# Kernel optimization log

Measured on AMD Instinct MI355X. Metric: run time of the kernel, lower is better.

## Reference

```python
import jax, jax.numpy as jnp
import numpy as np

B, T, C, H = 4, 2048, 768, 12
HD = C // H  # 64
EPS = 1e-5


def layer_norm(x, g, b):
    mu = jnp.mean(x, axis=-1, keepdims=True)
    var = jnp.var(x, axis=-1, keepdims=True)
    return (x - mu) * jax.lax.rsqrt(var + EPS) * g + b


def setup_inputs() -> dict:
    key = jax.random.key(0)
    ks = jax.random.split(key, 14)
    s_c = 1.0 / np.sqrt(C)
    s_4c = 1.0 / np.sqrt(4 * C)
    return {
        "x": jax.random.normal(ks[0], (B, T, C), jnp.float32),
        # per-head Q/K/V projections stacked over heads [H, C, HD]
        "wq": jax.random.uniform(ks[1], (H, C, HD), jnp.float32, -s_c, s_c),
        "bq": jnp.zeros((H, HD), jnp.float32),
        "wk": jax.random.uniform(ks[2], (H, C, HD), jnp.float32, -s_c, s_c),
        "bk": jnp.zeros((H, HD), jnp.float32),
        "wv": jax.random.uniform(ks[3], (H, C, HD), jnp.float32, -s_c, s_c),
        "bv": jnp.zeros((H, HD), jnp.float32),
        "w_proj": jax.random.uniform(ks[4], (C, C), jnp.float32, -s_c, s_c),
        "b_proj": jnp.zeros((C,), jnp.float32),
        "w1": jax.random.uniform(ks[5], (C, 4 * C), jnp.float32, -s_c, s_c),
        "b1": jnp.zeros((4 * C,), jnp.float32),
        "w2": jax.random.uniform(ks[6], (4 * C, C), jnp.float32, -s_4c, s_4c),
        "b2": jnp.zeros((C,), jnp.float32),
        "g1": jnp.ones((C,), jnp.float32),
        "beta1": jnp.zeros((C,), jnp.float32),
        "g2": jnp.ones((C,), jnp.float32),
        "beta2": jnp.zeros((C,), jnp.float32),
    }


def reference(x, wq, bq, wk, bk, wv, bv, w_proj, b_proj, w1, b1, w2, b2, g1, beta1, g2, beta2):
    # --- attention sublayer ---
    h = layer_norm(x, g1, beta1)
    q = jnp.einsum('btc,hcd->bhtd', h, wq) + bq[None, :, None, :]
    k = jnp.einsum('btc,hcd->bhtd', h, wk) + bk[None, :, None, :]
    v = jnp.einsum('btc,hcd->bhtd', h, wv) + bv[None, :, None, :]
    # NOTE: source applies NO 1/sqrt(head_size) scaling
    scores = jnp.einsum('bhtd,bhsd->bhts', q, k)  # [B,H,T,T]
    causal = jnp.tril(jnp.ones((T, T), bool))
    scores = jnp.where(causal, scores, -jnp.inf)
    wei = jax.nn.softmax(scores, axis=-1)
    attn = jnp.einsum('bhts,bhsd->bhtd', wei, v)  # [B,H,T,HD]
    attn = attn.transpose(0, 2, 1, 3).reshape(B, T, C)  # concat heads
    x = x + attn @ w_proj + b_proj
    # --- MLP sublayer ---
    h2 = layer_norm(x, g2, beta2)
    x = x + jax.nn.relu(h2 @ w1 + b1) @ w2 + b2
    return x
```

## Files before the change

### kernel.cpp

```cpp
#include <hip/hip_runtime.h>
#include <hip/hip_bf16.h>
#include <math.h>

#define BB 4
#define TT 2048
#define CC 768
#define HH 12
#define HDIM 64
#define C4 3072
#define MM (BB*TT)
#define EPSL 1e-5f

typedef __bf16 bf16x8 __attribute__((ext_vector_type(8)));
typedef __bf16 bf16x4 __attribute__((ext_vector_type(4)));
typedef float f32x4 __attribute__((ext_vector_type(4)));

__device__ __forceinline__ ushort f2bf(float f) {
    union { float f; unsigned u; } v; v.f = f;
    unsigned r = v.u + 0x7fffu + ((v.u >> 16) & 1u);
    return (ushort)(r >> 16);
}

__device__ __forceinline__ void glds16(const void* g, void* l) {
    __builtin_amdgcn_global_load_lds(
        (const __attribute__((address_space(1))) void*)g,
        (__attribute__((address_space(3))) void*)l, 16, 0, 0);
}

#define WVM(N) asm volatile("s_waitcnt vmcnt(" #N ")" ::: "memory")
#define WLG0   asm volatile("s_waitcnt lgkmcnt(0)" ::: "memory")

__device__ __forceinline__ void pbar() {
    __builtin_amdgcn_sched_barrier(0);
    __builtin_amdgcn_s_barrier();
    __builtin_amdgcn_sched_barrier(0);
}

__global__ __launch_bounds__(256) void ln_k(const float* __restrict__ X,
                                            const float* __restrict__ G,
                                            const float* __restrict__ Be,
                                            ushort* __restrict__ O)
{
    int row = blockIdx.x;
    const float* xr = X + (size_t)row * CC;
    int t = threadIdx.x;
    float v0 = xr[t], v1 = xr[t + 256], v2 = xr[t + 512];
    float s  = v0 + v1 + v2;
    float sq = v0*v0 + v1*v1 + v2*v2;
    #pragma unroll
    for (int off = 32; off; off >>= 1) {
        s  += __shfl_xor(s,  off);
        sq += __shfl_xor(sq, off);
    }
    __shared__ float red[8];
    int wv = t >> 6, ln = t & 63;
    if (ln == 0) { red[wv] = s; red[4 + wv] = sq; }
    __syncthreads();
    s  = red[0] + red[1] + red[2] + red[3];
    sq = red[4] + red[5] + red[6] + red[7];
    float mu  = s * (1.0f / CC);
    float var = sq * (1.0f / CC) - mu * mu;
    float rs  = rsqrtf(var + EPSL);
    ushort* orow = O + (size_t)row * CC;
    orow[t]       = f2bf((v0 - mu) * rs * G[t]       + Be[t]);
    orow[t + 256] = f2bf((v1 - mu) * rs * G[t + 256] + Be[t + 256]);
    orow[t + 512] = f2bf((v2 - mu) * rs * G[t + 512] + Be[t + 512]);
}

__global__ __launch_bounds__(256) void ln_add_k(float* __restrict__ X,
                                                const float* __restrict__ P,
                                                const float* __restrict__ G,
                                                const float* __restrict__ Be,
                                                ushort* __restrict__ O)
{
    int row = blockIdx.x;
    float* xr = X + (size_t)row * CC;
    const float* pr = P + (size_t)row * CC;
    int t = threadIdx.x;
    float v0 = xr[t]       + pr[t];
    float v1 = xr[t + 256] + pr[t + 256];
    float v2 = xr[t + 512] + pr[t + 512];
    xr[t] = v0; xr[t + 256] = v1; xr[t + 512] = v2;
    float s  = v0 + v1 + v2;
    float sq = v0*v0 + v1*v1 + v2*v2;
    #pragma unroll
    for (int off = 32; off; off >>= 1) {
        s  += __shfl_xor(s,  off);
        sq += __shfl_xor(sq, off);
    }
    __shared__ float red[8];
    int wv = t >> 6, ln = t & 63;
    if (ln == 0) { red[wv] = s; red[4 + wv] = sq; }
    __syncthreads();
    s  = red[0] + red[1] + red[2] + red[3];
    sq = red[4] + red[5] + red[6] + red[7];
    float mu  = s * (1.0f / CC);
    float var = sq * (1.0f / CC) - mu * mu;
    float rs  = rsqrtf(var + EPSL);
    ushort* orow = O + (size_t)row * CC;
    orow[t]       = f2bf((v0 - mu) * rs * G[t]       + Be[t]);
    orow[t + 256] = f2bf((v1 - mu) * rs * G[t + 256] + Be[t + 256]);
    orow[t + 512] = f2bf((v2 - mu) * rs * G[t + 512] + Be[t + 512]);
}

__global__ __launch_bounds__(256) void addto_k(float* __restrict__ o,
                                               const float* __restrict__ p,
                                               int n4)
{
    int i = blockIdx.x * 256 + threadIdx.x;
    int stride = gridDim.x * 256;
    for (; i < n4; i += stride) {
        float4 a = ((const float4*)o)[i];
        float4 b = ((const float4*)p)[i];
        a.x += b.x; a.y += b.y; a.z += b.z; a.w += b.w;
        ((float4*)o)[i] = a;
    }
}

__global__ __launch_bounds__(256) void repack_all_k(
    const float* __restrict__ wq, const float* __restrict__ wk,
    const float* __restrict__ wvw, const float* __restrict__ wp,
    const float* __restrict__ w1, const float* __restrict__ w2,
    ushort* __restrict__ WTqkv, ushort* __restrict__ WTp,
    ushort* __restrict__ WT1, ushort* __restrict__ WT2)
{
    __shared__ float tl[64][65];
    int blk = blockIdx.x;
    const float* W; ushort* WT;
    int N, outStride, nbx, local, mode;
    if (blk < 576) {
        int wsel = blk / 144; local = blk - wsel * 144; nbx = 12;
        N = 768; outStride = 768;
        mode = wsel < 3 ? 1 : 0;
        W  = wsel == 0 ? wq : (wsel == 1 ? wk : (wsel == 2 ? wvw : wp));
        WT = wsel == 3 ? WTp : WTqkv + (size_t)wsel * 768 * 768;
    } else if (blk < 1152) {
        local = blk - 576; nbx = 48; N = 3072; outStride = 768; mode = 0;
        W = w1; WT = WT1;
    } else {
        local = blk - 1152; nbx = 12; N = 768; outStride = 3072; mode = 0;
        W = w2; WT = WT2;
    }
    int n0 = (local % nbx) * 64, k0 = (local / nbx) * 64;
    int c = threadIdx.x & 63, rr = threadIdx.x >> 6;
    #pragma unroll
    for (int i = 0; i < 16; ++i) {
        int r = i * 4 + rr;
        float v;
        if (mode == 0) v = W[(size_t)(k0 + r) * N + n0 + c];
        else           v = W[((size_t)(n0 >> 6) * CC + k0 + r) * 64 + c];
        tl[r][c] = v;
    }
    __syncthreads();
    #pragma unroll
    for (int i = 0; i < 16; ++i) {
        int r = i * 4 + rr;
        WT[(size_t)(n0 + r) * outStride + k0 + c] = f2bf(tl[c][r]);
    }
}

template<int EPI>
__global__ __launch_bounds__(512, 3) void gemm3s(
    const ushort* __restrict__ A, const ushort* __restrict__ BT,
    int M, int N, int K,
    void* __restrict__ ov0, void* __restrict__ ov1, void* __restrict__ ov2,
    const float* __restrict__ bias0, const float* __restrict__ bias1,
    const float* __restrict__ bias2,
    const float* __restrict__ resid, ushort* __restrict__ obf,
    float* __restrict__ part)
{
    __shared__ ushort lds[3 * 12288];

    int nbx = gridDim.x;
    int nwg = nbx * gridDim.y * gridDim.z;
    int orig = (blockIdx.z * gridDim.y + blockIdx.y) * nbx + blockIdx.x;
    int cpx = nwg >> 3;
    int swz = (orig & 7) * cpx + (orig >> 3);
    int zi = swz / (nbx * gridDim.y);
    int rem = swz - zi * nbx * gridDim.y;
    int bn = rem % nbx, bm = rem / nbx;

    int tid = threadIdx.x;
    int lane = tid & 63;
    int w = tid >> 6;
    int wrow = (w >> 2) * 64, wcol = (w & 3) * 64;
    int fr = lane & 15, kh = lane >> 4;
    int rxor = ((fr >> 1) & 3) * 8;

    const size_t aR0 = (size_t)bm * 128;
    const size_t bR0 = (size_t)bn * 256;
    const int Ksl = K / (int)gridDim.z;
    const int koff = zi * Ksl;
    const int nt = Ksl >> 5;

    int srow = tid >> 2;
    int scol = (tid & 3) * 8;
    int sxor = scol ^ (((tid >> 3) & 3) * 8);

    f32x4 acc[4][4] = {};

    auto stage = [&](int slot, int t) {
        int kb = koff + (t << 5) + sxor;
        ushort* As = lds + slot * 12288;
        glds16(A  + (aR0 + srow) * K + kb,       As + srow * 32 + scol);
        glds16(BT + (bR0 + srow) * K + kb,       As + 4096 + srow * 32 + scol);
        glds16(BT + (bR0 + 128 + srow) * K + kb, As + 4096 + (128 + srow) * 32 + scol);
    };

    stage(0, 0);
    stage(1, 1);
    WVM(3);
    pbar();

    int slot = 0;
    for (int t = 0; t < nt; ++t) {
        const ushort* As = lds + slot * 12288;
        const ushort* Bs = As + 4096;
        bf16x8 aF[4], bF[4];
        #pragma unroll
        for (int i = 0; i < 4; ++i)
            aF[i] = *(const bf16x8*)&As[(wrow + i * 16 + fr) * 32 + ((kh * 8) ^ rxor)];
        #pragma unroll
        for (int j = 0; j < 4; ++j)
            bF[j] = *(const bf16x8*)&Bs[(wcol + j * 16 + fr) * 32 + ((kh * 8) ^ rxor)];
        if (t + 2 < nt) {
            int ns = slot + 2; if (ns >= 3) ns -= 3;
            stage(ns, t + 2);
        }
        __builtin_amdgcn_s_setprio(1);
        #pragma unroll
        for (int i = 0; i < 4; ++i)
            #pragma unroll
            for (int j = 0; j < 4; ++j)
                acc[i][j] = __builtin_amdgcn_mfma_f32_16x16x32_bf16(aF[i], bF[j], acc[i][j], 0, 0, 0);
        __builtin_amdgcn_s_setprio(0);
        if (t + 2 < nt) { WVM(3); } else { WVM(0); }
        WLG0;
        pbar();
        slot = slot + 1 == 3 ? 0 : slot + 1;
    }

    if (gridDim.z > 1 && zi > 0) {
        #pragma unroll
        for (int i = 0; i < 4; ++i) {
            int row0 = bm * 128 + wrow + i * 16 + kh * 4;
            #pragma unroll
            for (int j = 0; j < 4; ++j) {
                int col = bn * 256 + wcol + j * 16 + fr;
                #pragma unroll
                for (int r = 0; r < 4; ++r)
                    part[(size_t)(row0 + r) * N + col] = acc[i][j][r];
            }
        }
    } else if (EPI == 1) {
        int seg = bn / 3;
        ushort* op = (ushort*)(seg == 0 ? ov0 : (seg == 1 ? ov1 : ov2));
        const float* bsp = seg == 0 ? bias0 : (seg == 1 ? bias1 : bias2);
        int cb = (bn - seg * 3) * 256 + wcol;
        int h = cb >> 6;
        #pragma unroll
        for (int i = 0; i < 4; ++i) {
            int row0 = bm * 128 + wrow + i * 16 + kh * 4;
            int b = row0 >> 11;
            int t0 = row0 & (TT - 1);
            #pragma unroll
            for (int j = 0; j < 4; ++j) {
                int d = j * 16 + fr;
                float bsv = bsp[h * 64 + d];
                #pragma unroll
                for (int r = 0; r < 4; ++r)
                    op[((size_t)(b * HH + h) * TT + t0 + r) * 64 + d] =
                        f2bf(acc[i][j][r] + bsv);
            }
        }
    } else if (EPI == 2) {
        float* o0 = (float*)ov0;
        #pragma unroll
        for (int i = 0; i < 4; ++i) {
            int row0 = bm * 128 + wrow + i * 16 + kh * 4;
            #pragma unroll
            for (int j = 0; j < 4; ++j) {
                int col = bn * 256 + wcol + j * 16 + fr;
                float bsv = bias0[col];
                #pragma unroll
                for (int r = 0; r < 4; ++r) {
                    size_t idx = (size_t)(row0 + r) * N + col;
                    o0[idx] = acc[i][j][r] + bsv + resid[idx];
                }
            }
        }
    } else {
        #pragma unroll
        for (int i = 0; i < 4; ++i) {
            int row0 = bm * 128 + wrow + i * 16 + kh * 4;
            #pragma unroll
            for (int j = 0; j < 4; ++j) {
                int col = bn * 256 + wcol + j * 16 + fr;
                float bsv = bias0[col];
                #pragma unroll
                for (int r = 0; r < 4; ++r) {
                    float v = fmaxf(acc[i][j][r] + bsv, 0.f);
                    obf[(size_t)(row0 + r) * N + col] = f2bf(v);
                }
            }
        }
    }
}

__global__ __launch_bounds__(256) void vtrans_k(const ushort* __restrict__ V,
                                                ushort* __restrict__ Vt)
{
    __shared__ ushort tl[64][72];
    int blk = blockIdx.x;
    int tt = blk & 31, bh = blk >> 5;
    size_t base = (size_t)bh * TT * 64;
    int t0 = tt * 64;
    int e = threadIdx.x;
    int rr = e >> 3, cc8 = (e & 7) * 8;
    #pragma unroll
    for (int p = 0; p < 2; ++p) {
        int t = p * 32 + rr;
        *(uint4*)&tl[t][cc8] = *(const uint4*)&V[base + (size_t)(t0 + t) * 64 + cc8];
    }
    __syncthreads();
    #pragma unroll
    for (int p = 0; p < 2; ++p) {
        int d = p * 32 + rr;
        ushort tmp[8];
        #pragma unroll
        for (int i = 0; i < 8; ++i) tmp[i] = tl[cc8 + i][d];
        *(uint4*)&Vt[base + (size_t)d * TT + t0 + cc8] = *(uint4*)tmp;
    }
}

__global__ __launch_bounds__(256) void attn_k(const ushort* __restrict__ Q,
                                              const ushort* __restrict__ Kb,
                                              const ushort* __restrict__ Vt,
                                              ushort* __restrict__ Ob)
{
    __shared__ ushort Kl[2][64][64];
    __shared__ ushort Vl[2][64][64];
    __shared__ ushort Pl[4][16][68];

    int orig = blockIdx.x;
    int swz = (orig & 7) * 96 + (orig >> 3);
    int pair = swz & 15;
    int bh = swz >> 4;
    int b = bh / HH, h = bh - b * HH;
    int tid = threadIdx.x, lane = tid & 63, w = tid >> 6;
    int c = lane & 15, g = lane >> 4;
    size_t base = (size_t)bh * TT * 64;
    int srow = tid >> 3;
    int scol = (tid & 7) * 8;
    int sw0 = scol ^ ((srow & 7) * 8);
    int sw1 = scol ^ (((srow + 32) & 7) * 8);
    int rxk = (c & 7) * 8;
    const float LOG2E = 1.44269504088896340736f;

    #pragma unroll
    for (int sel = 0; sel < 2; ++sel) {
        int qt = sel ? (31 - pair) : pair;
        int q0 = qt * 64;
        int nt = qt + 1;

        bf16x8 aq[2];
        #pragma unroll
        for (int kc = 0; kc < 2; ++kc) {
            bf16x8 raw = *(const bf16x8*)&Q[base + (size_t)(q0 + w * 16 + c) * 64 + kc * 32 + g * 8];
            #pragma unroll
            for (int e = 0; e < 8; ++e)
                raw[e] = (__bf16)((float)raw[e] * LOG2E);
            aq[kc] = raw;
        }

        f32x4 oa[4] = {};
        float mrun[4] = {-INFINITY, -INFINITY, -INFINITY, -INFINITY};
        float lrun[4] = {0.f, 0.f, 0.f, 0.f};

        {
            uint4 a0 = *(const uint4*)&Kb[base + (size_t)srow * 64 + scol];
            uint4 a1 = *(const uint4*)&Kb[base + (size_t)(32 + srow) * 64 + scol];
            uint4 a2 = *(const uint4*)&Vt[base + (size_t)srow * TT + scol];
            uint4 a3 = *(const uint4*)&Vt[base + (size_t)(32 + srow) * TT + scol];
            *(uint4*)&Kl[0][srow][sw0]      = a0;
            *(uint4*)&Kl[0][32 + srow][sw1] = a1;
            *(uint4*)&Vl[0][srow][sw0]      = a2;
            *(uint4*)&Vl[0][32 + srow][sw1] = a3;
        }
        uint4 k0r, k1r, v0r, v1r;
        if (nt > 1) {
            k0r = *(const uint4*)&Kb[base + (size_t)(64 + srow) * 64 + scol];
            k1r = *(const uint4*)&Kb[base + (size_t)(96 + srow) * 64 + scol];
            v0r = *(const uint4*)&Vt[base + (size_t)srow * TT + 64 + scol];
            v1r = *(const uint4*)&Vt[base + (size_t)(32 + srow) * TT + 64 + scol];
        }
        __syncthreads();

        for (int t = 0; t < nt; ++t) {
            int cur = t & 1;
            if (t + 1 < nt) {
                int nxt = cur ^ 1;
                *(uint4*)&Kl[nxt][srow][sw0]      = k0r;
                *(uint4*)&Kl[nxt][32 + srow][sw1] = k1r;
                *(uint4*)&Vl[nxt][srow][sw0]      = v0r;
                *(uint4*)&Vl[nxt][32 + srow][sw1] = v1r;
                if (t + 2 < nt) {
                    int kn = (t + 2) * 64;
                    k0r = *(const uint4*)&Kb[base + (size_t)(kn + srow) * 64 + scol];
                    k1r = *(const uint4*)&Kb[base + (size_t)(kn + 32 + srow) * 64 + scol];
                    v0r = *(const uint4*)&Vt[base + (size_t)srow * TT + kn + scol];
                    v1r = *(const uint4*)&Vt[base + (size_t)(32 + srow) * TT + kn + scol];
                }
            }

            f32x4 sa[4] = {};
            #pragma unroll
            for (int kc = 0; kc < 2; ++kc)
                #pragma unroll
                for (int j = 0; j < 4; ++j) {
                    bf16x8 kf = *(const bf16x8*)&Kl[cur][j * 16 + c][(kc * 32 + g * 8) ^ rxk];
                    sa[j] = __builtin_amdgcn_mfma_f32_16x16x32_bf16(aq[kc], kf, sa[j], 0, 0, 0);
                }

            if (t == nt - 1) {
                #pragma unroll
                for (int j = 0; j < 4; ++j)
                    #pragma unroll
                    for (int r = 0; r < 4; ++r)
                        if (j * 16 + c > w * 16 + g * 4 + r) sa[j][r] = -1e30f;
            }

            float vlmax = sa[0][0];
            #pragma unroll
            for (int j = 0; j < 4; ++j)
                #pragma unroll
                for (int r = 0; r < 4; ++r) vlmax = fmaxf(vlmax, sa[j][r]);
            float mmin = fminf(fminf(mrun[0], mrun[1]), fminf(mrun[2], mrun[3]));
            if (!__all(vlmax <= mmin + 11.5f)) {
                #pragma unroll
                for (int r = 0; r < 4; ++r) {
                    float m0 = fmaxf(fmaxf(sa[0][r], sa[1][r]), fmaxf(sa[2][r], sa[3][r]));
                    #pragma unroll
                    for (int off = 8; off; off >>= 1) m0 = fmaxf(m0, __shfl_xor(m0, off));
                    float mnew = fmaxf(mrun[r], m0);
                    float sc = __builtin_amdgcn_exp2f(mrun[r] - mnew);
                    lrun[r] *= sc;
                    #pragma unroll
                    for (int j = 0; j < 4; ++j) oa[j][r] *= sc;
                    mrun[r] = mnew;
                }
            }
            #pragma unroll
            for (int r = 0; r < 4; ++r) {
                float ps = 0.f;
                #pragma unroll
                for (int j = 0; j < 4; ++j) {
                    float p = __builtin_amdgcn_exp2f(sa[j][r] - mrun[r]);
                    sa[j][r] = p;
                    ps += p;
                }
                lrun[r] += ps;
            }

            #pragma unroll
            for (int r = 0; r < 4; ++r)
                #pragma unroll
                for (int j = 0; j < 4; ++j)
                    Pl[w][g * 4 + r][j * 16 + c] = (ushort)__builtin_bit_cast(unsigned short, (__bf16)sa[j][r]);

            bf16x8 pf[2];
            #pragma unroll
            for (int kc = 0; kc < 2; ++kc) {
                bf16x4 lo = *(const bf16x4*)&Pl[w][c][kc * 32 + g * 8];
                bf16x4 hi = *(const bf16x4*)&Pl[w][c][kc * 32 + g * 8 + 4];
                pf[kc] = __builtin_shufflevector(lo, hi, 0, 1, 2, 3, 4, 5, 6, 7);
            }

            #pragma unroll
            for (int kc = 0; kc < 2; ++kc)
                #pragma unroll
                for (int j = 0; j < 4; ++j) {
                    bf16x8 vf = *(const bf16x8*)&Vl[cur][j * 16 + c][(kc * 32 + g * 8) ^ rxk];
                    oa[j] = __builtin_amdgcn_mfma_f32_16x16x32_bf16(pf[kc], vf, oa[j], 0, 0, 0);
                }

            __syncthreads();
        }

        float inv[4];
        #pragma unroll
        for (int r = 0; r < 4; ++r) {
            float l = lrun[r];
            #pragma unroll
            for (int off = 8; off; off >>= 1) l += __shfl_xor(l, off);
            inv[r] = 1.0f / l;
        }
        size_t orow = (size_t)b * TT + q0 + w * 16;
        #pragma unroll
        for (int j = 0; j < 4; ++j)
            #pragma unroll
            for (int r = 0; r < 4; ++r) {
                float v = oa[j][r] * inv[r];
                Ob[(orow + g * 4 + r) * CC + h * 64 + j * 16 + c] = f2bf(v);
            }
    }
}

extern "C" void kernel_launch(void* const* d_in, const int* in_sizes, int n_in,
                              void* d_out, int out_size, void* d_ws, size_t ws_size,
                              hipStream_t stream)
{
    const float* x   = (const float*)d_in[0];
    const float* wq  = (const float*)d_in[1];
    const float* bq  = (const float*)d_in[2];
    const float* wk  = (const float*)d_in[3];
    const float* bk  = (const float*)d_in[4];
    const float* wvw = (const float*)d_in[5];
    const float* bv  = (const float*)d_in[6];
    const float* wp  = (const float*)d_in[7];
    const float* bp  = (const float*)d_in[8];
    const float* w1  = (const float*)d_in[9];
    const float* b1  = (const float*)d_in[10];
    const float* w2  = (const float*)d_in[11];
    const float* b2  = (const float*)d_in[12];
    const float* g1  = (const float*)d_in[13];
    const float* be1 = (const float*)d_in[14];
    const float* g2  = (const float*)d_in[15];
    const float* be2 = (const float*)d_in[16];

    float* out = (float*)d_out;
    const size_t S = (size_t)MM * CC;

    ushort* wsu   = (ushort*)d_ws;
    ushort* WTqkv = wsu;
    ushort* WTp   = WTqkv + (size_t)2304 * 768;
    ushort* WT1   = WTp   + (size_t)768 * 768;
    ushort* WT2   = WT1   + (size_t)3072 * 768;
    ushort* hbf   = WT2   + (size_t)768 * 3072;
    ushort* attnb = hbf   + S;
    ushort* qb    = attnb + S;
    ushort* kb    = qb + S;
    ushort* vb    = kb + S;
    ushort* vtb   = vb + S;
    ushort* midb  = qb;
    float*  part_proj = (float*)qb;
    float*  part_w2   = (float*)hbf;

    repack_all_k<<<1728, 256, 0, stream>>>(wq, wk, wvw, wp, w1, w2,
                                           WTqkv, WTp, WT1, WT2);

    ln_k<<<MM, 256, 0, stream>>>(x, g1, be1, hbf);
    gemm3s<1><<<dim3(9, 64, 1), 512, 0, stream>>>(hbf, WTqkv, MM, 2304, CC,
        qb, kb, vb, bq, bk, bv, nullptr, nullptr, nullptr);
    vtrans_k<<<48 * 32, 256, 0, stream>>>(vb, vtb);
    attn_k<<<48 * 16, 256, 0, stream>>>(qb, kb, vtb, attnb);
    gemm3s<2><<<dim3(3, 64, 2), 512, 0, stream>>>(attnb, WTp, MM, CC, CC,
        out, nullptr, nullptr, bp, nullptr, nullptr, x, nullptr, part_proj);

    ln_add_k<<<MM, 256, 0, stream>>>(out, part_proj, g2, be2, hbf);
    gemm3s<3><<<dim3(12, 64, 1), 512, 0, stream>>>(hbf, WT1, MM, C4, CC,
        nullptr, nullptr, nullptr, b1, nullptr, nullptr, nullptr, midb, nullptr);
    gemm3s<2><<<dim3(3, 64, 2), 512, 0, stream>>>(midb, WT2, MM, CC, C4,
        out, nullptr, nullptr, b2, nullptr, nullptr, out, nullptr, part_w2);
    addto_k<<<2048, 256, 0, stream>>>(out, part_w2, MM * CC / 4);
}
```

Measured before the change: 280.3 us.

## Use 128-row query tiles with 8 waves per attention block

The attention kernel no longer pairs two 64-row query tiles inside each 256-thread block. Each 512-thread block now handles one 128-row query tile, longest tiles scheduled first, and its 8 waves share each K/V tile loaded into LDS. Waves whose rows lie entirely above a KV tile skip that tile's math, and masking is applied per wave. This halves the K/V load and sync overhead per query row. The cost is causal imbalance: early waves in a block idle through later KV tiles while the block's waves stay together on barriers.

New measurement: 284.2 us. No clear change (+1.4%).

```diff
diff --git a/kernel.cpp b/kernel.cpp
--- a/kernel.cpp
+++ b/kernel.cpp
@@ -333,86 +333,75 @@
     }
 }
 
-__global__ __launch_bounds__(256) void attn_k(const ushort* __restrict__ Q,
+__global__ __launch_bounds__(512) void attn_k(const ushort* __restrict__ Q,
                                               const ushort* __restrict__ Kb,
                                               const ushort* __restrict__ Vt,
                                               ushort* __restrict__ Ob)
 {
     __shared__ ushort Kl[2][64][64];
     __shared__ ushort Vl[2][64][64];
-    __shared__ ushort Pl[4][16][68];
+    __shared__ ushort Pl[8][16][68];
 
     int orig = blockIdx.x;
     int swz = (orig & 7) * 96 + (orig >> 3);
-    int pair = swz & 15;
     int bh = swz >> 4;
+    int qt = 15 - (swz & 15);
     int b = bh / HH, h = bh - b * HH;
+    int q0 = qt * 128;
+    int nt = 2 * qt + 2;
     int tid = threadIdx.x, lane = tid & 63, w = tid >> 6;
     int c = lane & 15, g = lane >> 4;
     size_t base = (size_t)bh * TT * 64;
     int srow = tid >> 3;
     int scol = (tid & 7) * 8;
-    int sw0 = scol ^ ((srow & 7) * 8);
-    int sw1 = scol ^ (((srow + 32) & 7) * 8);
+    int sw = scol ^ ((srow & 7) * 8);
     int rxk = (c & 7) * 8;
     const float LOG2E = 1.44269504088896340736f;
 
-    #pragma unroll
-    for (int sel = 0; sel < 2; ++sel) {
-        int qt = sel ? (31 - pair) : pair;
-        int q0 = qt * 64;
-        int nt = qt + 1;
-
-        bf16x8 aq[2];
-        #pragma unroll
-        for (int kc = 0; kc < 2; ++kc) {
-            bf16x8 raw = *(const bf16x8*)&Q[base + (size_t)(q0 + w * 16 + c) * 64 + kc * 32 + g * 8];
-            #pragma unroll
-            for (int e = 0; e < 8; ++e)
-                raw[e] = (__bf16)((float)raw[e] * LOG2E);
-            aq[kc] = raw;
-        }
-
-        f32x4 oa[4] = {};
-        float mrun[4] = {-INFINITY, -INFINITY, -INFINITY, -INFINITY};
-        float lrun[4] = {0.f, 0.f, 0.f, 0.f};
-
-        {
-            uint4 a0 = *(const uint4*)&Kb[base + (size_t)srow * 64 + scol];
-            uint4 a1 = *(const uint4*)&Kb[base + (size_t)(32 + srow) * 64 + scol];
-            uint4 a2 = *(const uint4*)&Vt[base + (size_t)srow * TT + scol];
-            uint4 a3 = *(const uint4*)&Vt[base + (size_t)(32 + srow) * TT + scol];
-            *(uint4*)&Kl[0][srow][sw0]      = a0;
-            *(uint4*)&Kl[0][32 + srow][sw1] = a1;
-            *(uint4*)&Vl[0][srow][sw0]      = a2;
-            *(uint4*)&Vl[0][32 + srow][sw1] = a3;
-        }
-        uint4 k0r, k1r, v0r, v1r;
-        if (nt > 1) {
-            k0r = *(const uint4*)&Kb[base + (size_t)(64 + srow) * 64 + scol];
-            k1r = *(const uint4*)&Kb[base + (size_t)(96 + srow) * 64 + scol];
-            v0r = *(const uint4*)&Vt[base + (size_t)srow * TT + 64 + scol];
-            v1r = *(const uint4*)&Vt[base + (size_t)(32 + srow) * TT + 64 + scol];
-        }
-        __syncthreads();
-
-        for (int t = 0; t < nt; ++t) {
-            int cur = t & 1;
-            if (t + 1 < nt) {
-                int nxt = cur ^ 1;
-                *(uint4*)&Kl[nxt][srow][sw0]      = k0r;
-                *(uint4*)&Kl[nxt][32 + srow][sw1] = k1r;
-                *(uint4*)&Vl[nxt][srow][sw0]      = v0r;
-                *(uint4*)&Vl[nxt][32 + srow][sw1] = v1r;
-                if (t + 2 < nt) {
-                    int kn = (t + 2) * 64;
-                    k0r = *(const uint4*)&Kb[base + (size_t)(kn + srow) * 64 + scol];
-                    k1r = *(const uint4*)&Kb[base + (size_t)(kn + 32 + srow) * 64 + scol];
-                    v0r = *(const uint4*)&Vt[base + (size_t)srow * TT + kn + scol];
-                    v1r = *(const uint4*)&Vt[base + (size_t)(32 + srow) * TT + kn + scol];
-                }
-            }
-
+    int wrow = w * 16;
+
+    bf16x8 aq[2];
+    #pragma unroll
+    for (int kc = 0; kc < 2; ++kc) {
+        bf16x8 raw = *(const bf16x8*)&Q[base + (size_t)(q0 + wrow + c) * 64 + kc * 32 + g * 8];
+        #pragma unroll
+        for (int e = 0; e < 8; ++e)
+            raw[e] = (__bf16)((float)raw[e] * LOG2E);
+        aq[kc] = raw;
+    }
+
+    f32x4 oa[4] = {};
+    float mrun[4] = {-INFINITY, -INFINITY, -INFINITY, -INFINITY};
+    float lrun[4] = {0.f, 0.f, 0.f, 0.f};
+
+    {
+        uint4 a0 = *(const uint4*)&Kb[base + (size_t)srow * 64 + scol];
+        uint4 a1 = *(const uint4*)&Vt[base + (size_t)srow * TT + scol];
+        *(uint4*)&Kl[0][srow][sw] = a0;
+        *(uint4*)&Vl[0][srow][sw] = a1;
+    }
+    uint4 kr, vr;
+    {
+        kr = *(const uint4*)&Kb[base + (size_t)(64 + srow) * 64 + scol];
+        vr = *(const uint4*)&Vt[base + (size_t)srow * TT + 64 + scol];
+    }
+    __syncthreads();
+
+    for (int t = 0; t < nt; ++t) {
+        int cur = t & 1;
+        int kv0 = t * 64;
+        if (t + 1 < nt) {
+            int nxt = cur ^ 1;
+            *(uint4*)&Kl[nxt][srow][sw] = kr;
+            *(uint4*)&Vl[nxt][srow][sw] = vr;
+            if (t + 2 < nt) {
+                int kn = (t + 2) * 64;
+                kr = *(const uint4*)&Kb[base + (size_t)(kn + srow) * 64 + scol];
+                vr = *(const uint4*)&Vt[base + (size_t)srow * TT + kn + scol];
+            }
+        }
+
+        if (kv0 <= q0 + wrow + 15) {
             f32x4 sa[4] = {};
             #pragma unroll
             for (int kc = 0; kc < 2; ++kc)
@@ -422,12 +411,12 @@
                     sa[j] = __builtin_amdgcn_mfma_f32_16x16x32_bf16(aq[kc], kf, sa[j], 0, 0, 0);
                 }
 
-            if (t == nt - 1) {
+            if (kv0 + 63 > q0 + wrow) {
                 #pragma unroll
                 for (int j = 0; j < 4; ++j)
                     #pragma unroll
                     for (int r = 0; r < 4; ++r)
-                        if (j * 16 + c > w * 16 + g * 4 + r) sa[j][r] = -1e30f;
+                        if (kv0 + j * 16 + c > q0 + wrow + g * 4 + r) sa[j][r] = -1e30f;
             }
 
             float vlmax = sa[0][0];
@@ -483,27 +472,27 @@
                     bf16x8 vf = *(const bf16x8*)&Vl[cur][j * 16 + c][(kc * 32 + g * 8) ^ rxk];
                     oa[j] = __builtin_amdgcn_mfma_f32_16x16x32_bf16(pf[kc], vf, oa[j], 0, 0, 0);
                 }
-
-            __syncthreads();
-        }
-
-        float inv[4];
+        }
+
+        __syncthreads();
+    }
+
+    float inv[4];
+    #pragma unroll
+    for (int r = 0; r < 4; ++r) {
+        float l = lrun[r];
+        #pragma unroll
+        for (int off = 8; off; off >>= 1) l += __shfl_xor(l, off);
+        inv[r] = 1.0f / l;
+    }
+    size_t orow = (size_t)b * TT + q0 + wrow;
+    #pragma unroll
+    for (int j = 0; j < 4; ++j)
         #pragma unroll
         for (int r = 0; r < 4; ++r) {
-            float l = lrun[r];
-            #pragma unroll
-            for (int off = 8; off; off >>= 1) l += __shfl_xor(l, off);
-            inv[r] = 1.0f / l;
-        }
-        size_t orow = (size_t)b * TT + q0 + w * 16;
-        #pragma unroll
-        for (int j = 0; j < 4; ++j)
-            #pragma unroll
-            for (int r = 0; r < 4; ++r) {
-                float v = oa[j][r] * inv[r];
-                Ob[(orow + g * 4 + r) * CC + h * 64 + j * 16 + c] = f2bf(v);
-            }
-    }
+            float v = oa[j][r] * inv[r];
+            Ob[(orow + g * 4 + r) * CC + h * 64 + j * 16 + c] = f2bf(v);
+        }
 }
 
 extern "C" void kernel_launch(void* const* d_in, const int* in_sizes, int n_in,
@@ -553,7 +542,7 @@
     gemm3s<1><<<dim3(9, 64, 1), 512, 0, stream>>>(hbf, WTqkv, MM, 2304, CC,
         qb, kb, vb, bq, bk, bv, nullptr, nullptr, nullptr);
     vtrans_k<<<48 * 32, 256, 0, stream>>>(vb, vtb);
-    attn_k<<<48 * 16, 256, 0, stream>>>(qb, kb, vtb, attnb);
+    attn_k<<<48 * 16, 512, 0, stream>>>(qb, kb, vtb, attnb);
     gemm3s<2><<<dim3(3, 64, 2), 512, 0, stream>>>(attnb, WTp, MM, CC, CC,
         out, nullptr, nullptr, bp, nullptr, nullptr, x, nullptr, part_proj);
 
```
